# Kernel optimization log

Hardware: AMD Instinct MI355X
Metric: run time of the kernel (lower is better)

The kernel has to match this reference:

```python
import jax, jax.numpy as jnp
import numpy as np

N_HEADS = 8   # n_heads
L = 2         # num_layers (= args.upper_T_num_layers)
H = 64        # hidden_size (= args.upper_T_hidden_dim)
F = 64        # input features
T = 12        # seq_len (= args.n_his)
N = 16384     # node_num (= LSTM batch dim)


def setup_inputs() -> dict:
    key = jax.random.key(0)
    ks = jax.random.split(key, 10)
    s = 0.05
    x = jax.random.normal(ks[0], (T, N, F), jnp.float32)
    # Stacked per-head, per-layer LSTM weights (PyTorch gate order: i, f, g, o).
    # Layer 0 input dim F == H so all layers stack cleanly.
    W_ih = jax.random.normal(ks[1], (L, N_HEADS, 4 * H, H), jnp.float32) * s
    W_hh = jax.random.normal(ks[2], (L, N_HEADS, 4 * H, H), jnp.float32) * s
    b_ih = jax.random.normal(ks[3], (L, N_HEADS, 4 * H), jnp.float32) * s
    b_hh = jax.random.normal(ks[4], (L, N_HEADS, 4 * H), jnp.float32) * s
    # Learned initial states (xavier-init nn.Parameters in the original).
    h0 = jax.random.normal(ks[5], (N_HEADS, L, N, H), jnp.float32) * s
    c0 = jax.random.normal(ks[6], (N_HEADS, L, N, H), jnp.float32) * s
    # 1x1 Conv2d(n_heads*n_his -> n_his): pure channel mixing.
    conv_w = jax.random.normal(ks[7], (T, N_HEADS * T), jnp.float32) * s
    conv_b = jax.random.normal(ks[8], (T,), jnp.float32) * s
    return {"x": x, "W_ih": W_ih, "W_hh": W_hh, "b_ih": b_ih, "b_hh": b_hh,
            "h0": h0, "c0": c0, "conv_w": conv_w, "conv_b": conv_b}


def _scan_lstm(gi, Whh, bhh, h0, c0):
    # gi: (T, heads, N, 4H) precomputed input contribution; h0/c0: (heads, N, H)
    def step(carry, g_t):
        h, c = carry
        gates = g_t + jnp.einsum('and,agd->ang', h, Whh) + bhh[:, None, :]
        i, f, g, o = jnp.split(gates, 4, axis=-1)
        c = jax.nn.sigmoid(f) * c + jax.nn.sigmoid(i) * jnp.tanh(g)
        h = jax.nn.sigmoid(o) * jnp.tanh(c)
        return (h, c), h
    (_, _), hs = jax.lax.scan(step, (h0, c0), gi)
    return hs  # (T, heads, N, H)


def reference(x, W_ih, W_hh, b_ih, b_hh, h0, c0, conv_w, conv_b):
    n_layers, n_heads = W_ih.shape[0], W_ih.shape[1]
    t_len, n_nodes, _ = x.shape
    hdim = W_hh.shape[-1]
    # Layer 0: input x is shared across heads; precompute input gates outside scan.
    gi = jnp.einsum('tnd,agd->tang', x, W_ih[0]) + b_ih[0][None, :, None, :]
    hs = _scan_lstm(gi, W_hh[0], b_hh[0], h0[:, 0], c0[:, 0])
    for l in range(1, n_layers):
        gi = jnp.einsum('tand,agd->tang', hs, W_ih[l]) + b_ih[l][None, :, None, :]
        hs = _scan_lstm(gi, W_hh[l], b_hh[l], h0[:, l], c0[:, l])
    # torch.cat over heads: head-major, then time -> channel dim = heads*T
    cat = jnp.transpose(hs, (1, 0, 2, 3)).reshape(n_heads * t_len, n_nodes, hdim)
    # 1x1 conv == channel mixing over (heads*T) -> T
    out = jnp.einsum('cnh,oc->onh', cat, conv_w) + conv_b[:, None, None]
    return out[None]  # (1, T, N, H)
```

## Files before the change

kernel.cpp:

```cpp
#include <hip/hip_runtime.h>
#include <hip/hip_bf16.h>


#define T_LEN 12
#define NHEADS 8
#define HD 64
#define NNODES 16384
#define MT 16
#define LDSP 72
#define WIH_ELEMS (2 * NHEADS * 4 * HD * HD)

typedef __bf16 bf16_t;
typedef __attribute__((ext_vector_type(2))) __bf16 bf16x2;
typedef __attribute__((ext_vector_type(4))) __bf16 bf16x4;
typedef __attribute__((ext_vector_type(8))) __bf16 bf16x8;
typedef __attribute__((ext_vector_type(2))) float f32x2;
typedef __attribute__((ext_vector_type(4))) float f32x4;

#define MFMA16(a, b, c) __builtin_amdgcn_mfma_f32_16x16x32_bf16((a), (b), (c), 0, 0, 0)

__device__ __forceinline__ float fast_sigmoid(float v) {
    return __builtin_amdgcn_rcpf(1.0f + __expf(-v));
}
__device__ __forceinline__ float fast_tanh(float v) {
    return 2.0f * __builtin_amdgcn_rcpf(1.0f + __expf(-2.0f * v)) - 1.0f;
}

__device__ __forceinline__ bf16x8 load8f(const float* p) {
    f32x4 a = *(const f32x4*)p;
    f32x4 b = *(const f32x4*)(p + 4);
    bf16x8 r;
    r[0] = (bf16_t)a[0]; r[1] = (bf16_t)a[1]; r[2] = (bf16_t)a[2]; r[3] = (bf16_t)a[3];
    r[4] = (bf16_t)b[0]; r[5] = (bf16_t)b[1]; r[6] = (bf16_t)b[2]; r[7] = (bf16_t)b[3];
    return r;
}
__device__ __forceinline__ bf16x4 load4f(const float* p) {
    f32x4 a = *(const f32x4*)p;
    bf16x4 r;
    r[0] = (bf16_t)a[0]; r[1] = (bf16_t)a[1]; r[2] = (bf16_t)a[2]; r[3] = (bf16_t)a[3];
    return r;
}

struct Gates { float sig_i, sig_f, tanh_g, sig_o; };
__device__ __forceinline__ Gates gate_eval(float gi, float gf, float gg, float go) {
    float ei = __expf(-gi), ef = __expf(-gf), eg = __expf(-2.0f * gg), eo = __expf(-go);
    float di = 1.0f + ei, df = 1.0f + ef, dg = 1.0f + eg, do_ = 1.0f + eo;
    float pif = di * df, pgo = dg * do_;
    float rr  = __builtin_amdgcn_rcpf(pif * pgo);
    float rif = rr * pgo, rgo = rr * pif;
    Gates g;
    g.sig_i  = rif * df;
    g.sig_f  = rif * di;
    g.tanh_g = 2.0f * (rgo * do_) - 1.0f;
    g.sig_o  = rgo * dg;
    return g;
}

__device__ __forceinline__ void tanh4(const float x[4], float out[4]) {
    float d0 = 1.0f + __expf(-2.0f * x[0]);
    float d1 = 1.0f + __expf(-2.0f * x[1]);
    float d2 = 1.0f + __expf(-2.0f * x[2]);
    float d3 = 1.0f + __expf(-2.0f * x[3]);
    float p01 = d0 * d1, p23 = d2 * d3;
    float rr  = __builtin_amdgcn_rcpf(p01 * p23);
    float r01 = rr * p23, r23 = rr * p01;
    out[0] = 2.0f * (r01 * d1) - 1.0f;
    out[1] = 2.0f * (r01 * d0) - 1.0f;
    out[2] = 2.0f * (r23 * d3) - 1.0f;
    out[3] = 2.0f * (r23 * d2) - 1.0f;
}

__device__ __forceinline__ void lstm_pointwise(const f32x4* acc, float* creg,
                                               bf16_t* D, int quad, int wq, int col) {
    float cn[4], so[4], tc[4];
    #pragma unroll
    for (int r = 0; r < 4; ++r) {
        Gates g = gate_eval(acc[0][r], acc[1][r], acc[2][r], acc[3][r]);
        cn[r] = g.sig_f * creg[r] + g.sig_i * g.tanh_g;
        so[r] = g.sig_o;
        creg[r] = cn[r];
    }
    tanh4(cn, tc);
    #pragma unroll
    for (int r = 0; r < 4; ++r)
        D[(quad * 4 + r) * LDSP + wq * 16 + col] = (bf16_t)(so[r] * tc[r]);
}

__global__ __launch_bounds__(256) void cvt_bf16_kernel(
    const float* __restrict__ src, bf16_t* __restrict__ dst, int n8)
{
    int i = blockIdx.x * 256 + threadIdx.x;
    if (i < n8) *(bf16x8*)(dst + (size_t)i * 8) = load8f(src + (size_t)i * 8);
}

template<bool PREP>
__global__ __launch_bounds__(512, 4) void lstm_pipe_kernel(
    const float* __restrict__ xg,
    const bf16_t* __restrict__ xbf,
    const float* __restrict__ Wih,
    const float* __restrict__ Whh,
    const bf16_t* __restrict__ wbf,
    const float* __restrict__ bih,
    const float* __restrict__ bhh,
    const float* __restrict__ h0g,
    const float* __restrict__ c0g,
    bf16_t* __restrict__ hsw)
{
    __shared__ __align__(16) bf16_t xT[T_LEN][MT][LDSP];
    __shared__ __align__(16) bf16_t h0A[2][MT][LDSP];
    __shared__ __align__(16) bf16_t h1A[2][MT][LDSP];

    const int tid  = threadIdx.x;
    const int w    = tid >> 6;
    const int lane = tid & 63;
    const int quad = lane >> 4;
    const int col  = lane & 15;
    const int lw   = w >> 2;
    const int wq   = w & 3;
    const int a    = blockIdx.x & (NHEADS - 1);
    const int nb   = (blockIdx.x >> 3) * MT;

    #pragma unroll
    for (int it = 0; it < 3; ++it) {
        int e    = (it * 512 + tid) * 8;
        int t    = e >> 10;
        int node = (e >> 6) & (MT - 1);
        int f    = e & (HD - 1);
        bf16x8 v;
        if (PREP) v = *(const bf16x8*)(xbf + ((size_t)t * NNODES + nb + node) * HD + f);
        else      v = load8f(xg + ((size_t)t * NNODES + nb + node) * HD + f);
        *(bf16x8*)&xT[t][node][f] = v;
    }
    {
        int e    = tid * 4;
        int l    = e >> 10;
        int node = (e >> 6) & (MT - 1);
        int hh   = e & (HD - 1);
        bf16x4 v = load4f(h0g + (((size_t)a * 2 + l) * NNODES + nb + node) * HD + hh);
        if (l == 0) *(bf16x4*)&h0A[0][node][hh] = v;
        else        *(bf16x4*)&h1A[1][node][hh] = v;
    }

    bf16x8 wA[4][2], wB[4][2];
    #pragma unroll
    for (int ni = 0; ni < 4; ++ni)
        #pragma unroll
        for (int kf = 0; kf < 2; ++kf) {
            size_t off = (((size_t)lw * NHEADS + a) * 256 + (4 * ni + wq) * 16 + col) * HD
                       + kf * 32 + quad * 8;
            if (PREP) {
                wA[ni][kf] = *(const bf16x8*)(wbf + off);
                wB[ni][kf] = *(const bf16x8*)(wbf + WIH_ELEMS + off);
            } else {
                wA[ni][kf] = load8f(Wih + off);
                wB[ni][kf] = load8f(Whh + off);
            }
        }
    float bias[4];
    #pragma unroll
    for (int ni = 0; ni < 4; ++ni) {
        int off = (lw * NHEADS + a) * 256 + ni * 64 + wq * 16 + col;
        bias[ni] = bih[off] + bhh[off];
    }
    float creg[4];
    #pragma unroll
    for (int r = 0; r < 4; ++r)
        creg[r] = c0g[(((size_t)a * 2 + lw) * NNODES + nb + quad * 4 + r) * HD
                      + wq * 16 + col];
    __syncthreads();

    int cur = 0;
    #pragma unroll 1
    for (int p = 0; p <= T_LEN; ++p) {
        if (p >= 2) {
            int node = tid >> 5;
            int h2   = (tid & 31) * 2;
            *(bf16x2*)(hsw + ((size_t)(a * T_LEN + p - 2) * NNODES + nb + node) * HD + h2) =
                *(const bf16x2*)&h1A[cur][node][h2];
        }
        const bool active = lw ? (p >= 1) : (p < T_LEN);
        if (active) {
            const bf16_t* P = lw ? &h0A[cur][0][0] : &xT[p][0][0];
            const bf16_t* Q = lw ? &h1A[cur][0][0] : &h0A[cur][0][0];
            bf16_t*       D = lw ? &h1A[cur ^ 1][0][0] : &h0A[cur ^ 1][0][0];
            const int ro = col * LDSP + quad * 8;
            bf16x8 a0 = *(const bf16x8*)(P + ro);
            bf16x8 b0 = *(const bf16x8*)(Q + ro);
            f32x4 acc[4];
            #pragma unroll
            for (int ni = 0; ni < 4; ++ni) {
                f32x4 z = {bias[ni], bias[ni], bias[ni], bias[ni]};
                z = MFMA16(a0, wA[ni][0], z);
                acc[ni] = MFMA16(b0, wB[ni][0], z);
            }
            bf16x8 a1 = *(const bf16x8*)(P + ro + 32);
            bf16x8 b1 = *(const bf16x8*)(Q + ro + 32);
            #pragma unroll
            for (int ni = 0; ni < 4; ++ni) {
                f32x4 z = MFMA16(a1, wA[ni][1], acc[ni]);
                acc[ni] = MFMA16(b1, wB[ni][1], z);
            }
            lstm_pointwise(acc, creg, D, quad, wq, col);
        }
        __syncthreads();
        cur ^= 1;
    }
    {
        int node = tid >> 5;
        int h2   = (tid & 31) * 2;
        *(bf16x2*)(hsw + ((size_t)(a * T_LEN + 11) * NNODES + nb + node) * HD + h2) =
            *(const bf16x2*)&h1A[cur][node][h2];
    }
}

__global__ __launch_bounds__(256, 8) void conv_reduce_kernel(
    const bf16_t* __restrict__ hsw,
    const float* __restrict__ cwg,
    const float* __restrict__ cbg,
    float* __restrict__ outg)
{
    int flat = blockIdx.x * 256 + threadIdx.x;
    int n  = flat >> 5;
    int h2 = (flat & 31) * 2;
    float a0[T_LEN], a1[T_LEN];
    #pragma unroll
    for (int o = 0; o < T_LEN; ++o) { float b = cbg[o]; a0[o] = b; a1[o] = b; }
    const bf16_t* src = hsw + (size_t)n * HD + h2;
    #pragma unroll 8
    for (int c = 0; c < NHEADS * T_LEN; ++c) {
        bf16x2 hv = *(const bf16x2*)(src + (size_t)c * NNODES * HD);
        float h0 = (float)hv[0], h1 = (float)hv[1];
        #pragma unroll
        for (int o = 0; o < T_LEN; ++o) {
            float cv = cwg[o * (NHEADS * T_LEN) + c];
            a0[o] += cv * h0;
            a1[o] += cv * h1;
        }
    }
    #pragma unroll
    for (int o = 0; o < T_LEN; ++o) {
        f32x2 v = {a0[o], a1[o]};
        *(f32x2*)(outg + ((size_t)o * NNODES + n) * HD + h2) = v;
    }
}

struct SmemT {
    __align__(16) bf16_t xT[T_LEN][MT][LDSP];
    __align__(16) bf16_t hA[2][2][MT][LDSP];
    __align__(16) float  cwf[T_LEN][NHEADS * T_LEN];
    __align__(16) float  cbf[T_LEN];
};

__global__ __launch_bounds__(256) void lstm_mono_kernel(
    const float* __restrict__ xg, const float* __restrict__ Wih,
    const float* __restrict__ Whh, const float* __restrict__ bih,
    const float* __restrict__ bhh, const float* __restrict__ h0g,
    const float* __restrict__ c0g, const float* __restrict__ cwg,
    const float* __restrict__ cbg, float* __restrict__ outg)
{
    __shared__ SmemT s;
    const int tid  = threadIdx.x;
    const int w    = tid >> 6;
    const int lane = tid & 63;
    const int quad = lane >> 4;
    const int col  = lane & 15;
    const int nb   = blockIdx.x * MT;

    #pragma unroll
    for (int it = 0; it < 6; ++it) {
        int ci   = it * 256 + tid;
        int e    = ci * 8;
        int t    = e >> 10;
        int node = (e >> 6) & (MT - 1);
        int f    = e & (HD - 1);
        *(bf16x8*)&s.xT[t][node][f] =
            load8f(xg + ((size_t)t * NNODES + nb + node) * HD + f);
    }
    for (int i = tid; i < T_LEN * NHEADS * T_LEN; i += 256)
        s.cwf[i / 96][i % 96] = cwg[i];
    if (tid < T_LEN) s.cbf[tid] = cbg[tid];

    float conv_acc[T_LEN][4];
    #pragma unroll
    for (int o = 0; o < T_LEN; ++o)
        #pragma unroll
        for (int r = 0; r < 4; ++r) conv_acc[o][r] = 0.0f;

    #pragma unroll 1
    for (int a = 0; a < NHEADS; ++a) {
        bf16x8 wih[2][4][2], whh[2][4][2];
        #pragma unroll
        for (int l = 0; l < 2; ++l)
            #pragma unroll
            for (int ni = 0; ni < 4; ++ni)
                #pragma unroll
                for (int kf = 0; kf < 2; ++kf) {
                    size_t off = (((size_t)l * NHEADS + a) * 256 + (4 * ni + w) * 16 + col) * HD
                               + kf * 32 + quad * 8;
                    wih[l][ni][kf] = load8f(Wih + off);
                    whh[l][ni][kf] = load8f(Whh + off);
                }
        float bias[2][4];
        #pragma unroll
        for (int l = 0; l < 2; ++l)
            #pragma unroll
            for (int ni = 0; ni < 4; ++ni) {
                int off = (l * NHEADS + a) * 256 + ni * 64 + w * 16 + col;
                bias[l][ni] = bih[off] + bhh[off];
            }
        float creg[2][4];
        #pragma unroll
        for (int l = 0; l < 2; ++l)
            #pragma unroll
            for (int r = 0; r < 4; ++r)
                creg[l][r] = c0g[(((size_t)a * 2 + l) * NNODES + nb + quad * 4 + r) * HD
                                 + w * 16 + col];
        {
            int e    = tid * 8;
            int l    = e >> 10;
            int node = (e >> 6) & (MT - 1);
            int hh   = e & (HD - 1);
            *(bf16x8*)&s.hA[l][0][node][hh] =
                load8f(h0g + (((size_t)a * 2 + l) * NNODES + nb + node) * HD + hh);
        }
        __syncthreads();

        int cur = 0;
        #pragma unroll 1
        for (int t = 0; t < T_LEN; ++t) {
            bf16x8 xa0 = *(const bf16x8*)&s.xT[t][col][quad * 8];
            bf16x8 xa1 = *(const bf16x8*)&s.xT[t][col][32 + quad * 8];
            bf16x8 ha0 = *(const bf16x8*)&s.hA[0][cur][col][quad * 8];
            bf16x8 ha1 = *(const bf16x8*)&s.hA[0][cur][col][32 + quad * 8];
            f32x4 acc[4];
            #pragma unroll
            for (int ni = 0; ni < 4; ++ni) {
                f32x4 z = {0.f, 0.f, 0.f, 0.f};
                z = MFMA16(xa0, wih[0][ni][0], z);
                z = MFMA16(xa1, wih[0][ni][1], z);
                z = MFMA16(ha0, whh[0][ni][0], z);
                z = MFMA16(ha1, whh[0][ni][1], z);
                acc[ni] = z;
            }
            #pragma unroll
            for (int r = 0; r < 4; ++r) {
                float ig = fast_sigmoid(acc[0][r] + bias[0][0]);
                float fg = fast_sigmoid(acc[1][r] + bias[0][1]);
                float gg = fast_tanh   (acc[2][r] + bias[0][2]);
                float og = fast_sigmoid(acc[3][r] + bias[0][3]);
                float cn = fg * creg[0][r] + ig * gg;
                creg[0][r] = cn;
                s.hA[0][cur ^ 1][quad * 4 + r][w * 16 + col] = (bf16_t)(og * fast_tanh(cn));
            }
            __syncthreads();
            bf16x8 pa0 = *(const bf16x8*)&s.hA[0][cur ^ 1][col][quad * 8];
            bf16x8 pa1 = *(const bf16x8*)&s.hA[0][cur ^ 1][col][32 + quad * 8];
            bf16x8 qa0 = *(const bf16x8*)&s.hA[1][cur][col][quad * 8];
            bf16x8 qa1 = *(const bf16x8*)&s.hA[1][cur][col][32 + quad * 8];
            #pragma unroll
            for (int ni = 0; ni < 4; ++ni) {
                f32x4 z = {0.f, 0.f, 0.f, 0.f};
                z = MFMA16(pa0, wih[1][ni][0], z);
                z = MFMA16(pa1, wih[1][ni][1], z);
                z = MFMA16(qa0, whh[1][ni][0], z);
                z = MFMA16(qa1, whh[1][ni][1], z);
                acc[ni] = z;
            }
            float hn[4];
            #pragma unroll
            for (int r = 0; r < 4; ++r) {
                float ig = fast_sigmoid(acc[0][r] + bias[1][0]);
                float fg = fast_sigmoid(acc[1][r] + bias[1][1]);
                float gg = fast_tanh   (acc[2][r] + bias[1][2]);
                float og = fast_sigmoid(acc[3][r] + bias[1][3]);
                float cn = fg * creg[1][r] + ig * gg;
                creg[1][r] = cn;
                hn[r] = og * fast_tanh(cn);
                s.hA[1][cur ^ 1][quad * 4 + r][w * 16 + col] = (bf16_t)hn[r];
            }
            #pragma unroll
            for (int o = 0; o < T_LEN; ++o) {
                float cv = s.cwf[o][a * T_LEN + t];
                #pragma unroll
                for (int r = 0; r < 4; ++r) conv_acc[o][r] += cv * hn[r];
            }
            __syncthreads();
            cur ^= 1;
        }
    }
    #pragma unroll
    for (int o = 0; o < T_LEN; ++o)
        #pragma unroll
        for (int r = 0; r < 4; ++r)
            outg[((size_t)o * NNODES + nb + quad * 4 + r) * HD + w * 16 + col] =
                conv_acc[o][r] + s.cbf[o];
}

extern "C" void kernel_launch(void* const* d_in, const int* in_sizes, int n_in,
                              void* d_out, int out_size, void* d_ws, size_t ws_size,
                              hipStream_t stream) {
    (void)in_sizes; (void)n_in; (void)out_size;
    const float* x   = (const float*)d_in[0];
    const float* Wih = (const float*)d_in[1];
    const float* Whh = (const float*)d_in[2];
    const float* bih = (const float*)d_in[3];
    const float* bhh = (const float*)d_in[4];
    const float* h0  = (const float*)d_in[5];
    const float* c0  = (const float*)d_in[6];
    const float* cw  = (const float*)d_in[7];
    const float* cb  = (const float*)d_in[8];
    const size_t hs_bytes = (size_t)NHEADS * T_LEN * NNODES * HD * sizeof(bf16_t);
    const size_t x_bytes  = (size_t)T_LEN * NNODES * HD * sizeof(bf16_t);
    const size_t w_bytes  = (size_t)2 * WIH_ELEMS * sizeof(bf16_t);
    if (ws_size >= hs_bytes + x_bytes + w_bytes) {
        bf16_t* hs  = (bf16_t*)d_ws;
        bf16_t* xbf = (bf16_t*)((char*)d_ws + hs_bytes);
        bf16_t* wbf = (bf16_t*)((char*)d_ws + hs_bytes + x_bytes);
        const int n8x = T_LEN * NNODES * HD / 8;
        const int n8w = WIH_ELEMS / 8;
        cvt_bf16_kernel<<<dim3(n8x / 256), dim3(256), 0, stream>>>(x, xbf, n8x);
        cvt_bf16_kernel<<<dim3((n8w + 255) / 256), dim3(256), 0, stream>>>(Wih, wbf, n8w);
        cvt_bf16_kernel<<<dim3((n8w + 255) / 256), dim3(256), 0, stream>>>(Whh, wbf + WIH_ELEMS, n8w);
        lstm_pipe_kernel<true><<<dim3((NNODES / MT) * NHEADS), dim3(512), 0, stream>>>(
            x, xbf, Wih, Whh, wbf, bih, bhh, h0, c0, hs);
        conv_reduce_kernel<<<dim3(NNODES * 32 / 256), dim3(256), 0, stream>>>(
            hs, cw, cb, (float*)d_out);
    } else if (ws_size >= hs_bytes) {
        bf16_t* hs = (bf16_t*)d_ws;
        lstm_pipe_kernel<false><<<dim3((NNODES / MT) * NHEADS), dim3(512), 0, stream>>>(
            x, nullptr, Wih, Whh, nullptr, bih, bhh, h0, c0, hs);
        conv_reduce_kernel<<<dim3(NNODES * 32 / 256), dim3(256), 0, stream>>>(
            hs, cw, cb, (float*)d_out);
    } else {
        lstm_mono_kernel<<<dim3(NNODES / MT), dim3(256), 0, stream>>>(
            x, Wih, Whh, bih, bhh, h0, c0, cw, cb, (float*)d_out);
    }
}
```

Before: 548.1 us.

## Prescale LSTM weights for exp2 gates, transpose MFMA, write hs directly

Weights and biases are pre-multiplied by log2(e) (and 2·log2(e) for the g gate) during bf16 conversion, so gate activations use raw exp2 with no per-element scaling. MFMA operands are swapped so each lane owns 4 contiguous hidden units of one node. That lets h be stored as a bf16x4 vector to LDS and straight to global hs, replacing the separate per-step copy-out pass. Bias moves into LDS as vector loads, c0 is loaded as a vector, and the conv reduce kernel now processes 4 hidden elements per thread. Rounding the prescaled weights to bf16 slightly changes numerics.

Measured after the change: 533.7 us. -2.6%, faster.

```diff
diff --git a/kernel.cpp b/kernel.cpp
--- a/kernel.cpp
+++ b/kernel.cpp
@@ -14,10 +14,15 @@
 typedef __attribute__((ext_vector_type(2))) __bf16 bf16x2;
 typedef __attribute__((ext_vector_type(4))) __bf16 bf16x4;
 typedef __attribute__((ext_vector_type(8))) __bf16 bf16x8;
-typedef __attribute__((ext_vector_type(2))) float f32x2;
 typedef __attribute__((ext_vector_type(4))) float f32x4;
 
 #define MFMA16(a, b, c) __builtin_amdgcn_mfma_f32_16x16x32_bf16((a), (b), (c), 0, 0, 0)
+
+#if __has_builtin(__builtin_amdgcn_exp2f)
+#define EXP2(x) __builtin_amdgcn_exp2f(x)
+#else
+#define EXP2(x) exp2f(x)
+#endif
 
 __device__ __forceinline__ float fast_sigmoid(float v) {
     return __builtin_amdgcn_rcpf(1.0f + __expf(-v));
@@ -41,49 +46,48 @@
     return r;
 }
 
-struct Gates { float sig_i, sig_f, tanh_g, sig_o; };
-__device__ __forceinline__ Gates gate_eval(float gi, float gf, float gg, float go) {
-    float ei = __expf(-gi), ef = __expf(-gf), eg = __expf(-2.0f * gg), eo = __expf(-go);
-    float di = 1.0f + ei, df = 1.0f + ef, dg = 1.0f + eg, do_ = 1.0f + eo;
-    float pif = di * df, pgo = dg * do_;
-    float rr  = __builtin_amdgcn_rcpf(pif * pgo);
-    float rif = rr * pgo, rgo = rr * pif;
-    Gates g;
-    g.sig_i  = rif * df;
-    g.sig_f  = rif * di;
-    g.tanh_g = 2.0f * (rgo * do_) - 1.0f;
-    g.sig_o  = rgo * dg;
-    return g;
-}
-
-__device__ __forceinline__ void tanh4(const float x[4], float out[4]) {
-    float d0 = 1.0f + __expf(-2.0f * x[0]);
-    float d1 = 1.0f + __expf(-2.0f * x[1]);
-    float d2 = 1.0f + __expf(-2.0f * x[2]);
-    float d3 = 1.0f + __expf(-2.0f * x[3]);
+template<bool SC>
+__device__ __forceinline__ bf16x4 lstm_pointwise_sw(const f32x4* acc, float* creg) {
+    float cn[4], so[4], tc[4];
+    #pragma unroll
+    for (int r = 0; r < 4; ++r) {
+        float ei, ef, eg, eo;
+        if (SC) {
+            ei = EXP2(-acc[0][r]); ef = EXP2(-acc[1][r]);
+            eg = EXP2(-acc[2][r]); eo = EXP2(-acc[3][r]);
+        } else {
+            ei = __expf(-acc[0][r]); ef = __expf(-acc[1][r]);
+            eg = __expf(-2.0f * acc[2][r]); eo = __expf(-acc[3][r]);
+        }
+        float di = 1.0f + ei, df = 1.0f + ef, dg = 1.0f + eg, do_ = 1.0f + eo;
+        float pif = di * df, pgo = dg * do_;
+        float rr  = __builtin_amdgcn_rcpf(pif * pgo);
+        float rif = rr * pgo, rgo = rr * pif;
+        float sig_i  = rif * df;
+        float sig_f  = rif * di;
+        float tanh_g = 2.0f * (rgo * do_) - 1.0f;
+        so[r] = rgo * dg;
+        float cnr = sig_f * creg[r] + sig_i * tanh_g;
+        cn[r] = cnr;
+        creg[r] = cnr;
+    }
+    float d0 = 1.0f + EXP2(cn[0] * -2.885390082f);
+    float d1 = 1.0f + EXP2(cn[1] * -2.885390082f);
+    float d2 = 1.0f + EXP2(cn[2] * -2.885390082f);
+    float d3 = 1.0f + EXP2(cn[3] * -2.885390082f);
     float p01 = d0 * d1, p23 = d2 * d3;
     float rr  = __builtin_amdgcn_rcpf(p01 * p23);
     float r01 = rr * p23, r23 = rr * p01;
-    out[0] = 2.0f * (r01 * d1) - 1.0f;
-    out[1] = 2.0f * (r01 * d0) - 1.0f;
-    out[2] = 2.0f * (r23 * d3) - 1.0f;
-    out[3] = 2.0f * (r23 * d2) - 1.0f;
-}
-
-__device__ __forceinline__ void lstm_pointwise(const f32x4* acc, float* creg,
-                                               bf16_t* D, int quad, int wq, int col) {
-    float cn[4], so[4], tc[4];
-    #pragma unroll
-    for (int r = 0; r < 4; ++r) {
-        Gates g = gate_eval(acc[0][r], acc[1][r], acc[2][r], acc[3][r]);
-        cn[r] = g.sig_f * creg[r] + g.sig_i * g.tanh_g;
-        so[r] = g.sig_o;
-        creg[r] = cn[r];
-    }
-    tanh4(cn, tc);
-    #pragma unroll
-    for (int r = 0; r < 4; ++r)
-        D[(quad * 4 + r) * LDSP + wq * 16 + col] = (bf16_t)(so[r] * tc[r]);
+    tc[0] = 2.0f * (r01 * d1) - 1.0f;
+    tc[1] = 2.0f * (r01 * d0) - 1.0f;
+    tc[2] = 2.0f * (r23 * d3) - 1.0f;
+    tc[3] = 2.0f * (r23 * d2) - 1.0f;
+    bf16x4 hv;
+    hv[0] = (bf16_t)(so[0] * tc[0]);
+    hv[1] = (bf16_t)(so[1] * tc[1]);
+    hv[2] = (bf16_t)(so[2] * tc[2]);
+    hv[3] = (bf16_t)(so[3] * tc[3]);
+    return hv;
 }
 
 __global__ __launch_bounds__(256) void cvt_bf16_kernel(
@@ -91,6 +95,25 @@
 {
     int i = blockIdx.x * 256 + threadIdx.x;
     if (i < n8) *(bf16x8*)(dst + (size_t)i * 8) = load8f(src + (size_t)i * 8);
+}
+
+__global__ __launch_bounds__(256) void cvt_w_kernel(
+    const float* __restrict__ src, bf16_t* __restrict__ dst, int n8)
+{
+    int i = blockIdx.x * 256 + threadIdx.x;
+    if (i >= n8) return;
+    int row  = (i >> 3) & 255;
+    int gate = row >> 6;
+    float sc = (gate == 2) ? 2.885390082f : 1.442695041f;
+    const float* p = src + (size_t)i * 8;
+    f32x4 a = *(const f32x4*)p;
+    f32x4 b = *(const f32x4*)(p + 4);
+    bf16x8 r;
+    r[0] = (bf16_t)(a[0]*sc); r[1] = (bf16_t)(a[1]*sc);
+    r[2] = (bf16_t)(a[2]*sc); r[3] = (bf16_t)(a[3]*sc);
+    r[4] = (bf16_t)(b[0]*sc); r[5] = (bf16_t)(b[1]*sc);
+    r[6] = (bf16_t)(b[2]*sc); r[7] = (bf16_t)(b[3]*sc);
+    *(bf16x8*)(dst + (size_t)i * 8) = r;
 }
 
 template<bool PREP>
@@ -109,6 +132,7 @@
     __shared__ __align__(16) bf16_t xT[T_LEN][MT][LDSP];
     __shared__ __align__(16) bf16_t h0A[2][MT][LDSP];
     __shared__ __align__(16) bf16_t h1A[2][MT][LDSP];
+    __shared__ __align__(16) float  biasLds[2][4][4][16];
 
     const int tid  = threadIdx.x;
     const int w    = tid >> 6;
@@ -140,6 +164,16 @@
         if (l == 0) *(bf16x4*)&h0A[0][node][hh] = v;
         else        *(bf16x4*)&h1A[1][node][hh] = v;
     }
+    {
+        int l   = tid >> 8;
+        int r   = tid & 255;
+        int wqi = r >> 6;
+        int nii = (r >> 4) & 3;
+        int gc  = r & 15;
+        int off = (l * NHEADS + a) * 256 + nii * 64 + wqi * 16 + gc;
+        float sc = PREP ? (nii == 2 ? 2.885390082f : 1.442695041f) : 1.0f;
+        biasLds[l][wqi][nii][gc] = (bih[off] + bhh[off]) * sc;
+    }
 
     bf16x8 wA[4][2], wB[4][2];
     #pragma unroll
@@ -156,28 +190,17 @@
                 wB[ni][kf] = load8f(Whh + off);
             }
         }
-    float bias[4];
-    #pragma unroll
-    for (int ni = 0; ni < 4; ++ni) {
-        int off = (lw * NHEADS + a) * 256 + ni * 64 + wq * 16 + col;
-        bias[ni] = bih[off] + bhh[off];
-    }
     float creg[4];
-    #pragma unroll
-    for (int r = 0; r < 4; ++r)
-        creg[r] = c0g[(((size_t)a * 2 + lw) * NNODES + nb + quad * 4 + r) * HD
-                      + wq * 16 + col];
+    {
+        f32x4 cv = *(const f32x4*)(c0g + (((size_t)a * 2 + lw) * NNODES + nb + col) * HD
+                                   + wq * 16 + quad * 4);
+        creg[0] = cv[0]; creg[1] = cv[1]; creg[2] = cv[2]; creg[3] = cv[3];
+    }
     __syncthreads();
 
     int cur = 0;
     #pragma unroll 1
     for (int p = 0; p <= T_LEN; ++p) {
-        if (p >= 2) {
-            int node = tid >> 5;
-            int h2   = (tid & 31) * 2;
-            *(bf16x2*)(hsw + ((size_t)(a * T_LEN + p - 2) * NNODES + nb + node) * HD + h2) =
-                *(const bf16x2*)&h1A[cur][node][h2];
-        }
         const bool active = lw ? (p >= 1) : (p < T_LEN);
         if (active) {
             const bf16_t* P = lw ? &h0A[cur][0][0] : &xT[p][0][0];
@@ -189,59 +212,58 @@
             f32x4 acc[4];
             #pragma unroll
             for (int ni = 0; ni < 4; ++ni) {
-                f32x4 z = {bias[ni], bias[ni], bias[ni], bias[ni]};
-                z = MFMA16(a0, wA[ni][0], z);
-                acc[ni] = MFMA16(b0, wB[ni][0], z);
+                f32x4 z = *(const f32x4*)&biasLds[lw][wq][ni][quad * 4];
+                z = MFMA16(wA[ni][0], a0, z);
+                acc[ni] = MFMA16(wB[ni][0], b0, z);
             }
             bf16x8 a1 = *(const bf16x8*)(P + ro + 32);
             bf16x8 b1 = *(const bf16x8*)(Q + ro + 32);
             #pragma unroll
             for (int ni = 0; ni < 4; ++ni) {
-                f32x4 z = MFMA16(a1, wA[ni][1], acc[ni]);
-                acc[ni] = MFMA16(b1, wB[ni][1], z);
-            }
-            lstm_pointwise(acc, creg, D, quad, wq, col);
+                f32x4 z = MFMA16(wA[ni][1], a1, acc[ni]);
+                acc[ni] = MFMA16(wB[ni][1], b1, z);
+            }
+            bf16x4 hv = lstm_pointwise_sw<PREP>(acc, creg);
+            *(bf16x4*)(D + col * LDSP + wq * 16 + quad * 4) = hv;
+            if (lw)
+                *(bf16x4*)(hsw + ((size_t)(a * T_LEN + (p - 1)) * NNODES + nb + col) * HD
+                           + wq * 16 + quad * 4) = hv;
         }
         __syncthreads();
         cur ^= 1;
     }
-    {
-        int node = tid >> 5;
-        int h2   = (tid & 31) * 2;
-        *(bf16x2*)(hsw + ((size_t)(a * T_LEN + 11) * NNODES + nb + node) * HD + h2) =
-            *(const bf16x2*)&h1A[cur][node][h2];
-    }
-}
-
-__global__ __launch_bounds__(256, 8) void conv_reduce_kernel(
+}
+
+__global__ __launch_bounds__(256) void conv_reduce_kernel(
     const bf16_t* __restrict__ hsw,
     const float* __restrict__ cwg,
     const float* __restrict__ cbg,
     float* __restrict__ outg)
 {
     int flat = blockIdx.x * 256 + threadIdx.x;
-    int n  = flat >> 5;
-    int h2 = (flat & 31) * 2;
-    float a0[T_LEN], a1[T_LEN];
-    #pragma unroll
-    for (int o = 0; o < T_LEN; ++o) { float b = cbg[o]; a0[o] = b; a1[o] = b; }
-    const bf16_t* src = hsw + (size_t)n * HD + h2;
-    #pragma unroll 8
+    int n  = flat >> 4;
+    int h4 = (flat & 15) * 4;
+    f32x4 acc[T_LEN];
+    #pragma unroll
+    for (int o = 0; o < T_LEN; ++o) {
+        float b = cbg[o];
+        acc[o][0] = b; acc[o][1] = b; acc[o][2] = b; acc[o][3] = b;
+    }
+    const bf16_t* src = hsw + (size_t)n * HD + h4;
+    #pragma unroll 6
     for (int c = 0; c < NHEADS * T_LEN; ++c) {
-        bf16x2 hv = *(const bf16x2*)(src + (size_t)c * NNODES * HD);
-        float h0 = (float)hv[0], h1 = (float)hv[1];
+        bf16x4 hv = *(const bf16x4*)(src + (size_t)c * NNODES * HD);
+        float h0 = (float)hv[0], h1 = (float)hv[1], h2 = (float)hv[2], h3 = (float)hv[3];
         #pragma unroll
         for (int o = 0; o < T_LEN; ++o) {
             float cv = cwg[o * (NHEADS * T_LEN) + c];
-            a0[o] += cv * h0;
-            a1[o] += cv * h1;
-        }
-    }
-    #pragma unroll
-    for (int o = 0; o < T_LEN; ++o) {
-        f32x2 v = {a0[o], a1[o]};
-        *(f32x2*)(outg + ((size_t)o * NNODES + n) * HD + h2) = v;
-    }
+            acc[o][0] += cv * h0; acc[o][1] += cv * h1;
+            acc[o][2] += cv * h2; acc[o][3] += cv * h3;
+        }
+    }
+    #pragma unroll
+    for (int o = 0; o < T_LEN; ++o)
+        *(f32x4*)(outg + ((size_t)o * NNODES + n) * HD + h4) = acc[o];
 }
 
 struct SmemT {
@@ -419,17 +441,17 @@
         const int n8x = T_LEN * NNODES * HD / 8;
         const int n8w = WIH_ELEMS / 8;
         cvt_bf16_kernel<<<dim3(n8x / 256), dim3(256), 0, stream>>>(x, xbf, n8x);
-        cvt_bf16_kernel<<<dim3((n8w + 255) / 256), dim3(256), 0, stream>>>(Wih, wbf, n8w);
-        cvt_bf16_kernel<<<dim3((n8w + 255) / 256), dim3(256), 0, stream>>>(Whh, wbf + WIH_ELEMS, n8w);
+        cvt_w_kernel<<<dim3((n8w + 255) / 256), dim3(256), 0, stream>>>(Wih, wbf, n8w);
+        cvt_w_kernel<<<dim3((n8w + 255) / 256), dim3(256), 0, stream>>>(Whh, wbf + WIH_ELEMS, n8w);
         lstm_pipe_kernel<true><<<dim3((NNODES / MT) * NHEADS), dim3(512), 0, stream>>>(
             x, xbf, Wih, Whh, wbf, bih, bhh, h0, c0, hs);
-        conv_reduce_kernel<<<dim3(NNODES * 32 / 256), dim3(256), 0, stream>>>(
+        conv_reduce_kernel<<<dim3(NNODES * 16 / 256), dim3(256), 0, stream>>>(
             hs, cw, cb, (float*)d_out);
     } else if (ws_size >= hs_bytes) {
         bf16_t* hs = (bf16_t*)d_ws;
         lstm_pipe_kernel<false><<<dim3((NNODES / MT) * NHEADS), dim3(512), 0, stream>>>(
             x, nullptr, Wih, Whh, nullptr, bih, bhh, h0, c0, hs);
-        conv_reduce_kernel<<<dim3(NNODES * 32 / 256), dim3(256), 0, stream>>>(
+        conv_reduce_kernel<<<dim3(NNODES * 16 / 256), dim3(256), 0, stream>>>(
             hs, cw, cb, (float*)d_out);
     } else {
         lstm_mono_kernel<<<dim3(NNODES / MT), dim3(256), 0, stream>>>(
```
